# Performance work log

Measured on AMD Instinct MI355X. Metric: run time of the kernel, lower is better.

## Reference

```python
import jax, jax.numpy as jnp
import numpy as np

FILTER_WIDTH = 6


def setup_inputs() -> dict:
    key = jax.random.key(0)
    ks = jax.random.split(key, 9)
    V, E, H, C = 50000, 128, 128, 2
    B, S = 64, 512
    inputs = jax.random.randint(ks[0], (B, S), 0, V)
    lengths = jax.random.randint(ks[1], (B,), 1, S)
    embed_table = (jax.random.normal(ks[2], (V, E), jnp.float32) * 0.1).at[0].set(0.0)  # padding_idx=0
    s = 1.0 / np.sqrt(H)
    w_ih = jax.random.uniform(ks[3], (4 * H, E), jnp.float32, -s, s)
    w_hh = jax.random.uniform(ks[4], (4 * H, H), jnp.float32, -s, s)
    b_ih = jax.random.uniform(ks[5], (4 * H,), jnp.float32, -s, s)
    b_hh = jax.random.uniform(ks[6], (4 * H,), jnp.float32, -s, s)
    sf = 1.0 / np.sqrt(H)
    fc_w = jax.random.uniform(ks[7], (C, H), jnp.float32, -sf, sf)
    fc_b = jax.random.uniform(ks[8], (C,), jnp.float32, -sf, sf)
    return dict(inputs=inputs, lengths=lengths, embed_table=embed_table,
                w_ih=w_ih, w_hh=w_hh, b_ih=b_ih, b_hh=b_hh, fc_w=fc_w, fc_b=fc_b)


def reference(inputs, lengths, embed_table, w_ih, w_hh, b_ih, b_hh, fc_w, fc_b):
    # Dropouts are identity in eval mode (p set to 0).
    B, S = inputs.shape
    E = embed_table.shape[1]
    H = w_hh.shape[1]
    FW = FILTER_WIDTH
    W = S - FW + 1

    emb = embed_table[inputs]                                   # [B, S, E]
    idx = jnp.arange(W)[:, None] + jnp.arange(FW)[None, :]       # [W, FW]
    xw = emb[:, idx, :]                                          # [B, W, FW, E] sliding windows
    x = xw.reshape(B * W, FW, E).transpose(1, 0, 2)              # [FW, B*W, E] time-major

    bias = b_ih + b_hh

    def step(carry, xt):
        h, c = carry
        g = xt @ w_ih.T + h @ w_hh.T + bias                      # [B*W, 4H], gate order i,f,g,o
        i, f, gg, o = jnp.split(g, 4, axis=-1)
        c = jax.nn.sigmoid(f) * c + jax.nn.sigmoid(i) * jnp.tanh(gg)
        h = jax.nn.sigmoid(o) * jnp.tanh(c)
        return (h, c), None

    h0 = jnp.zeros((B * W, H), emb.dtype)
    (h_last, _), _ = jax.lax.scan(step, (h0, h0), x)             # final hidden per window
    feat = jnp.max(h_last.reshape(B, W, H), axis=1)              # max-pool over windows
    return feat @ fc_w.T + fc_b                                  # [B, num_class]
```

## Files before the change

kernel.cpp:

```cpp
#include <hip/hip_runtime.h>
#include <math.h>
#include <float.h>

#define Bn   64
#define Sn   512
#define FWn  6
#define Wn   507
#define WT   32
#define NTILE 16

#define PROWS   37
#define PSTRIDE 512

typedef __attribute__((ext_vector_type(8))) _Float16 half8;
typedef __attribute__((ext_vector_type(4))) _Float16 half4;
typedef __attribute__((ext_vector_type(4))) float f32x4;

__device__ __forceinline__ float sigf(float x)  {
    return __builtin_amdgcn_rcpf(1.0f + __expf(-x));
}
__device__ __forceinline__ float tanh_(float x) {
    return 1.0f - 2.0f * __builtin_amdgcn_rcpf(__expf(2.0f * x) + 1.0f);
}

__global__ void __launch_bounds__(256)
pack_w_kernel(const float* __restrict__ w_ih, const float* __restrict__ w_hh,
              _Float16* __restrict__ wih_p, _Float16* __restrict__ whh_p)
{
    const int idx = blockIdx.x * 256 + threadIdx.x;
    const int j  = idx & 7;
    const int L  = (idx >> 3) & 63;
    const int ks = (idx >> 9) & 3;
    const int nt = idx >> 11;
    const int row = nt * 16 + (L & 15);
    const int col = ks * 32 + (L >> 4) * 8 + j;
    wih_p[idx] = (_Float16)w_ih[row * 128 + col];
    whh_p[idx] = (_Float16)w_hh[row * 128 + col];
}

__global__ void __launch_bounds__(512)
lstm_kernel(const int* __restrict__ inputs, const float* __restrict__ embed,
            const _Float16* __restrict__ wih_p, const _Float16* __restrict__ whh_p,
            const float* __restrict__ b_ih, const float* __restrict__ b_hh,
            float* __restrict__ partial)
{
    __shared__ __align__(16) _Float16 Pt[PROWS * PSTRIDE];
    __shared__ __align__(16) _Float16 hsA[2][2][2048];
    const int t    = threadIdx.x;
    const int L    = t & 63;
    const int ut   = t >> 6;
    const int b    = blockIdx.x >> 4;
    const int tile = blockIdx.x & 15;
    const int w0   = tile * WT;
    const int q  = L >> 4;
    const int ln = L & 15;
    const int j8 = L & 7;
    const int u  = ut * 16 + ln;

    {
        f32x4 accx[3][4];
#pragma unroll
        for (int g = 0; g < 4; ++g) {
            const float bg = b_ih[g * 128 + u] + b_hh[g * 128 + u];
            accx[0][g] = (f32x4){bg, bg, bg, bg};
            accx[1][g] = accx[0][g];
            accx[2][g] = accx[0][g];
        }
        int tok[3];
#pragma unroll
        for (int mt = 0; mt < 3; ++mt) {
            int s = w0 + mt * 16 + ln; s = s < 511 ? s : 511;
            tok[mt] = inputs[b * Sn + s];
        }
#pragma unroll
        for (int ks = 0; ks < 4; ++ks) {
            half8 ax[3];
#pragma unroll
            for (int mt = 0; mt < 3; ++mt) {
                const float* er = embed + (size_t)tok[mt] * 128 + ks * 32 + q * 8;
                float4 e0 = *(const float4*)er;
                float4 e1 = *(const float4*)(er + 4);
                half8 a;
                a[0] = (_Float16)e0.x; a[1] = (_Float16)e0.y;
                a[2] = (_Float16)e0.z; a[3] = (_Float16)e0.w;
                a[4] = (_Float16)e1.x; a[5] = (_Float16)e1.y;
                a[6] = (_Float16)e1.z; a[7] = (_Float16)e1.w;
                ax[mt] = a;
            }
#pragma unroll
            for (int g = 0; g < 4; ++g) {
                half8 bw = *(const half8*)(wih_p + ((size_t)((g * 8 + ut) * 4 + ks) * 64 + L) * 8);
#pragma unroll
                for (int mt = 0; mt < 3; ++mt)
                    accx[mt][g] = __builtin_amdgcn_mfma_f32_16x16x32_f16(ax[mt], bw, accx[mt][g], 0, 0, 0);
            }
        }
#pragma unroll
        for (int mt = 0; mt < 3; ++mt)
#pragma unroll
            for (int r = 0; r < 4; ++r) {
                const int sl = mt * 16 + q * 4 + r;
                if (sl < PROWS) {
                    half4 o;
                    o[0] = (_Float16)accx[mt][0][r];
                    o[1] = (_Float16)accx[mt][1][r];
                    o[2] = (_Float16)accx[mt][2][r];
                    o[3] = (_Float16)accx[mt][3][r];
                    *(half4*)&Pt[sl * PSTRIDE + u * 4] = o;
                }
            }
    }

    half8 whf[4][4];
#pragma unroll
    for (int g = 0; g < 4; ++g)
#pragma unroll
        for (int ks = 0; ks < 4; ++ks)
            whf[g][ks] = *(const half8*)(whh_p + ((size_t)((g * 8 + ut) * 4 + ks) * 64 + L) * 8);

    __syncthreads();

    const int ks_h = ut >> 1;
    const int qp   = (ut & 1) * 2 + (ln >> 3);

    float cst[2][4] = {{0.f, 0.f, 0.f, 0.f}, {0.f, 0.f, 0.f, 0.f}};
    float hh[2][4];

    for (int st = 0; st < FWn; ++st) {
        if (st > 0) __syncthreads();
#pragma unroll
        for (int sub = 0; sub < 2; ++sub) {
            f32x4 acc[4];
#pragma unroll
            for (int r = 0; r < 4; ++r) {
                half4 pv = *(const half4*)&Pt[(sub * 16 + q * 4 + r + st) * PSTRIDE + u * 4];
                acc[0][r] = (float)pv[0]; acc[1][r] = (float)pv[1];
                acc[2][r] = (float)pv[2]; acc[3][r] = (float)pv[3];
            }
            if (st > 0) {
                const _Float16* hb = hsA[(st + 1) & 1][sub];
#pragma unroll
                for (int ks = 0; ks < 4; ++ks) {
                    half8 ah = *(const half8*)(hb + (ks * 64 + L) * 8);
#pragma unroll
                    for (int g = 0; g < 4; ++g)
                        acc[g] = __builtin_amdgcn_mfma_f32_16x16x32_f16(ah, whf[g][ks], acc[g], 0, 0, 0);
                }
            }
            _Float16* buf = hsA[st & 1][sub];
#pragma unroll
            for (int r = 0; r < 4; ++r) {
                float ii = sigf(acc[0][r]);
                float ff = sigf(acc[1][r]);
                float gg = tanh_(acc[2][r]);
                float oo = sigf(acc[3][r]);
                float cc = ff * cst[sub][r] + ii * gg;
                cst[sub][r] = cc;
                hh[sub][r] = oo * tanh_(cc);
                if (st < FWn - 1)
                    buf[ks_h * 512 + (qp * 16 + q * 4 + r) * 8 + j8] = (_Float16)hh[sub][r];
            }
        }
    }

    float mv = -FLT_MAX;
#pragma unroll
    for (int sub = 0; sub < 2; ++sub)
#pragma unroll
        for (int r = 0; r < 4; ++r) {
            const int w = w0 + sub * 16 + q * 4 + r;
            if (w < Wn) mv = fmaxf(mv, hh[sub][r]);
        }
    mv = fmaxf(mv, __shfl_xor(mv, 16));
    mv = fmaxf(mv, __shfl_xor(mv, 32));
    if (q == 0)
        partial[(size_t)(b * NTILE + tile) * 128 + u] = mv;
}

__global__ void __launch_bounds__(128)
final_kernel(const float* __restrict__ partial, const float* __restrict__ fc_w,
             const float* __restrict__ fc_b, float* __restrict__ out)
{
    const int b = blockIdx.x;
    const int u = threadIdx.x;
    float m = -FLT_MAX;
#pragma unroll
    for (int tl = 0; tl < NTILE; ++tl)
        m = fmaxf(m, partial[(size_t)(b * NTILE + tl) * 128 + u]);
    float v0 = m * fc_w[u];
    float v1 = m * fc_w[128 + u];
#pragma unroll
    for (int off = 1; off < 64; off <<= 1) {
        v0 += __shfl_xor(v0, off);
        v1 += __shfl_xor(v1, off);
    }
    __shared__ float red[2][2];
    if ((u & 63) == 0) { red[u >> 6][0] = v0; red[u >> 6][1] = v1; }
    __syncthreads();
    if (u == 0) {
        out[b * 2 + 0] = red[0][0] + red[1][0] + fc_b[0];
        out[b * 2 + 1] = red[0][1] + red[1][1] + fc_b[1];
    }
}

extern "C" void kernel_launch(void* const* d_in, const int* in_sizes, int n_in,
                              void* d_out, int out_size, void* d_ws, size_t ws_size,
                              hipStream_t stream)
{
    const int*   inputs = (const int*)d_in[0];
    const float* embed  = (const float*)d_in[2];
    const float* w_ih   = (const float*)d_in[3];
    const float* w_hh   = (const float*)d_in[4];
    const float* b_ih   = (const float*)d_in[5];
    const float* b_hh   = (const float*)d_in[6];
    const float* fc_w   = (const float*)d_in[7];
    const float* fc_b   = (const float*)d_in[8];
    float* out = (float*)d_out;

    float*    partial = (float*)d_ws;
    _Float16* wih_p   = (_Float16*)(partial + Bn * NTILE * 128);
    _Float16* whh_p   = wih_p + 65536;

    pack_w_kernel<<<dim3(256), 256, 0, stream>>>(w_ih, w_hh, wih_p, whh_p);
    lstm_kernel<<<dim3(Bn * NTILE), 512, 0, stream>>>(inputs, embed, wih_p, whh_p,
                                                      b_ih, b_hh, partial);
    final_kernel<<<dim3(Bn), 128, 0, stream>>>(partial, fc_w, fc_b, out);
}
```

Baseline: 154.6 us.

## Cut register pressure: reorder input projection loop and stream W_hh from global

Reorders the input-projection loop so each 16-row M tile is finished before the next, which keeps only 4 accumulators live instead of 12. The recurrent W_hh fragments are no longer held in registers for the whole kernel; they are reloaded from global memory (L2-resident) at each MFMA. A launch bound of 8 is added to push for higher occupancy. In exchange, the recurrent loop now issues many repeated global loads on its critical path. The fp16 weight fragments are also reread once per M tile.

```diff
diff --git a/kernel.cpp b/kernel.cpp
--- a/kernel.cpp
+++ b/kernel.cpp
@@ -38,7 +38,7 @@
     whh_p[idx] = (_Float16)w_hh[row * 128 + col];
 }
 
-__global__ void __launch_bounds__(512)
+__global__ void __launch_bounds__(512, 8)
 lstm_kernel(const int* __restrict__ inputs, const float* __restrict__ embed,
             const _Float16* __restrict__ wih_p, const _Float16* __restrict__ whh_p,
             const float* __restrict__ b_ih, const float* __restrict__ b_hh,
@@ -58,14 +58,10 @@
     const int u  = ut * 16 + ln;
 
     {
-        f32x4 accx[3][4];
-#pragma unroll
-        for (int g = 0; g < 4; ++g) {
-            const float bg = b_ih[g * 128 + u] + b_hh[g * 128 + u];
-            accx[0][g] = (f32x4){bg, bg, bg, bg};
-            accx[1][g] = accx[0][g];
-            accx[2][g] = accx[0][g];
-        }
+        float bg[4];
+#pragma unroll
+        for (int g = 0; g < 4; ++g)
+            bg[g] = b_ih[g * 128 + u] + b_hh[g * 128 + u];
         int tok[3];
 #pragma unroll
         for (int mt = 0; mt < 3; ++mt) {
@@ -73,10 +69,13 @@
             tok[mt] = inputs[b * Sn + s];
         }
 #pragma unroll
-        for (int ks = 0; ks < 4; ++ks) {
-            half8 ax[3];
-#pragma unroll
-            for (int mt = 0; mt < 3; ++mt) {
+        for (int mt = 0; mt < 3; ++mt) {
+            f32x4 acc[4];
+#pragma unroll
+            for (int g = 0; g < 4; ++g)
+                acc[g] = (f32x4){bg[g], bg[g], bg[g], bg[g]};
+#pragma unroll
+            for (int ks = 0; ks < 4; ++ks) {
                 const float* er = embed + (size_t)tok[mt] * 128 + ks * 32 + q * 8;
                 float4 e0 = *(const float4*)er;
                 float4 e1 = *(const float4*)(er + 4);
@@ -85,38 +84,26 @@
                 a[2] = (_Float16)e0.z; a[3] = (_Float16)e0.w;
                 a[4] = (_Float16)e1.x; a[5] = (_Float16)e1.y;
                 a[6] = (_Float16)e1.z; a[7] = (_Float16)e1.w;
-                ax[mt] = a;
-            }
-#pragma unroll
-            for (int g = 0; g < 4; ++g) {
-                half8 bw = *(const half8*)(wih_p + ((size_t)((g * 8 + ut) * 4 + ks) * 64 + L) * 8);
-#pragma unroll
-                for (int mt = 0; mt < 3; ++mt)
-                    accx[mt][g] = __builtin_amdgcn_mfma_f32_16x16x32_f16(ax[mt], bw, accx[mt][g], 0, 0, 0);
-            }
-        }
-#pragma unroll
-        for (int mt = 0; mt < 3; ++mt)
+#pragma unroll
+                for (int g = 0; g < 4; ++g) {
+                    half8 bw = *(const half8*)(wih_p + ((size_t)((g * 8 + ut) * 4 + ks) * 64 + L) * 8);
+                    acc[g] = __builtin_amdgcn_mfma_f32_16x16x32_f16(a, bw, acc[g], 0, 0, 0);
+                }
+            }
 #pragma unroll
             for (int r = 0; r < 4; ++r) {
                 const int sl = mt * 16 + q * 4 + r;
                 if (sl < PROWS) {
                     half4 o;
-                    o[0] = (_Float16)accx[mt][0][r];
-                    o[1] = (_Float16)accx[mt][1][r];
-                    o[2] = (_Float16)accx[mt][2][r];
-                    o[3] = (_Float16)accx[mt][3][r];
+                    o[0] = (_Float16)acc[0][r];
+                    o[1] = (_Float16)acc[1][r];
+                    o[2] = (_Float16)acc[2][r];
+                    o[3] = (_Float16)acc[3][r];
                     *(half4*)&Pt[sl * PSTRIDE + u * 4] = o;
                 }
             }
-    }
-
-    half8 whf[4][4];
-#pragma unroll
-    for (int g = 0; g < 4; ++g)
-#pragma unroll
-        for (int ks = 0; ks < 4; ++ks)
-            whf[g][ks] = *(const half8*)(whh_p + ((size_t)((g * 8 + ut) * 4 + ks) * 64 + L) * 8);
+        }
+    }
 
     __syncthreads();
 
@@ -143,8 +130,10 @@
                 for (int ks = 0; ks < 4; ++ks) {
                     half8 ah = *(const half8*)(hb + (ks * 64 + L) * 8);
 #pragma unroll
-                    for (int g = 0; g < 4; ++g)
-                        acc[g] = __builtin_amdgcn_mfma_f32_16x16x32_f16(ah, whf[g][ks], acc[g], 0, 0, 0);
+                    for (int g = 0; g < 4; ++g) {
+                        half8 bw = *(const half8*)(whh_p + ((size_t)((g * 8 + ut) * 4 + ks) * 64 + L) * 8);
+                        acc[g] = __builtin_amdgcn_mfma_f32_16x16x32_f16(ah, bw, acc[g], 0, 0, 0);
+                    }
                 }
             }
             _Float16* buf = hsA[st & 1][sub];
```

After: 175.8 us. +13.7%, slower.
